# Kernel optimization log

Measured on AMD Instinct MI355X. Metric: run time of the kernel, lower is better.

Reference implementation:

```python
import math
import jax, jax.numpy as jnp
import numpy as np

D_MODEL = 1024
D_STATE = 16
D_CONV = 4
EXPAND = 2
D_INNER = EXPAND * D_MODEL
DT_RANK = max(1, math.ceil(D_MODEL / 16))
B_SZ, L_SEQ = 2, 2048


def setup_inputs() -> dict:
    key = jax.random.key(0)
    ks = jax.random.split(key, 8)
    s = 0.02
    x = jax.random.normal(ks[0], (B_SZ, L_SEQ, D_MODEL), dtype=jnp.float32)
    W_in = jax.random.normal(ks[1], (2 * D_INNER, D_MODEL), dtype=jnp.float32) * s
    conv_w = jax.random.normal(ks[2], (D_INNER, 1, D_CONV), dtype=jnp.float32) * s
    conv_b = jax.random.normal(ks[3], (D_INNER,), dtype=jnp.float32) * s
    W_xproj = jax.random.normal(ks[4], (DT_RANK + 2 * D_STATE, D_INNER), dtype=jnp.float32) * s
    W_dt = jax.random.normal(ks[5], (D_INNER, DT_RANK), dtype=jnp.float32) * s
    b_dt = jax.random.normal(ks[6], (D_INNER,), dtype=jnp.float32) * s
    A_log = jnp.broadcast_to(jnp.log(jnp.arange(1, D_STATE + 1, dtype=jnp.float32))[None, :], (D_INNER, D_STATE))
    D = jnp.ones((D_INNER,), dtype=jnp.float32)
    W_out = jax.random.normal(ks[7], (D_MODEL, D_INNER), dtype=jnp.float32) * s
    return {"x": x, "W_in": W_in, "conv_w": conv_w, "conv_b": conv_b,
            "W_xproj": W_xproj, "W_dt": W_dt, "b_dt": b_dt,
            "A_log": A_log, "D": D, "W_out": W_out}


def _silu(v):
    return v * jax.nn.sigmoid(v)


def _selective_scan(xc, dt, A, Bm, Cm):
    # xc, dt: (B, L, d_inner); A: (d_inner, N); Bm, Cm: (B, L, N)
    batch = xc.shape[0]
    h0 = jnp.zeros((batch, D_INNER, D_STATE), dtype=xc.dtype)

    def step(h, inp):
        x_t, dt_t, B_t, C_t = inp  # (B,d_inner), (B,d_inner), (B,N), (B,N)
        A_bar = jnp.exp(dt_t[:, :, None] * A[None])            # (B, d_inner, N)
        h = A_bar * h + (dt_t * x_t)[:, :, None] * B_t[:, None, :]
        y_t = jnp.einsum('bdn,bn->bd', h, C_t)
        return h, y_t

    xs = (jnp.swapaxes(xc, 0, 1), jnp.swapaxes(dt, 0, 1),
          jnp.swapaxes(Bm, 0, 1), jnp.swapaxes(Cm, 0, 1))
    _, ys = jax.lax.scan(step, h0, xs)  # ys: (L, B, d_inner)
    return jnp.swapaxes(ys, 0, 1)


def reference(x, W_in, conv_w, conv_b, W_xproj, W_dt, b_dt, A_log, D, W_out):
    # in_proj
    xz = jnp.einsum('bld,ed->ble', x, W_in)                    # (B, L, 2*d_inner)
    xc, z = jnp.split(xz, 2, axis=-1)
    # causal depthwise conv1d (torch pads d_conv-1 both sides then truncates to L)
    xc_ncl = jnp.swapaxes(xc, 1, 2)                            # (B, d_inner, L)
    xc_ncl = jax.lax.conv_general_dilated(
        xc_ncl, conv_w, window_strides=(1,), padding=[(D_CONV - 1, 0)],
        dimension_numbers=('NCH', 'OIH', 'NCH'), feature_group_count=D_INNER)
    xc_ncl = xc_ncl + conv_b[None, :, None]
    xc = _silu(jnp.swapaxes(xc_ncl, 1, 2))                     # (B, L, d_inner)
    # input-dependent dt, B, C
    xp = jnp.einsum('bld,ed->ble', xc, W_xproj)
    dt_lr = xp[:, :, :DT_RANK]
    Bm = xp[:, :, DT_RANK:DT_RANK + D_STATE]
    Cm = xp[:, :, DT_RANK + D_STATE:]
    dt = jax.nn.softplus(jnp.einsum('blr,dr->bld', dt_lr, W_dt) + b_dt)
    A = -jnp.exp(A_log)                                        # (d_inner, N)
    y = _selective_scan(xc, dt, A, Bm, Cm)
    y = y + xc * D[None, None, :]
    y = y * _silu(z)
    return jnp.einsum('bld,od->blo', y, W_out)
```

## Files before the change

kernel.cpp:

```cpp
#include <hip/hip_runtime.h>
#include <cstddef>
#include <cstdint>

#define DMODEL 1024
#define DI     2048
#define LSEQ   2048
#define NB     2
#define DSTATE 16
#define DTRANK 64
#define NXP    96
#define MROWS  (NB*LSEQ)
#define CHUNKS 32
#define LC     (LSEQ/CHUNKS)

typedef __attribute__((ext_vector_type(8))) short bf16x8;
typedef __attribute__((ext_vector_type(8))) unsigned short u16x8;
typedef __attribute__((ext_vector_type(4))) float f32x4;

__device__ __forceinline__ float silu_f(float v) {
  return v / (1.f + __expf(-v));
}
__device__ __forceinline__ float softplus_f(float v) {
  return (v > 20.f) ? v : log1pf(__expf(v));
}
__device__ __forceinline__ unsigned short f2bf(float f) {
  unsigned u = __float_as_uint(f);
  unsigned r = (u + 0x7FFFu + ((u >> 16) & 1u)) >> 16;
  return (unsigned short)r;
}
__device__ __forceinline__ float bf2f(unsigned short h) {
  return __uint_as_float(((unsigned)h) << 16);
}
__device__ __forceinline__ void gl2lds16(const void* g, void* l) {
  __builtin_amdgcn_global_load_lds(
      (const __attribute__((address_space(1))) void*)g,
      (__attribute__((address_space(3))) void*)l, 16, 0, 0);
}

__global__ __launch_bounds__(256)
void prep_kernel(const float* __restrict__ W_in, const float* __restrict__ W_dt,
                 const float* __restrict__ W_out, const float* __restrict__ x,
                 const float* __restrict__ W_xproj,
                 unsigned short* __restrict__ Whi, unsigned short* __restrict__ Wlo,
                 unsigned short* __restrict__ wdhi, unsigned short* __restrict__ wdlo,
                 unsigned short* __restrict__ Wohi, unsigned short* __restrict__ Wolo,
                 unsigned short* __restrict__ xhi, unsigned short* __restrict__ xlo,
                 unsigned short* __restrict__ wxhi, unsigned short* __restrict__ wxlo,
                 float* __restrict__ xp, float* __restrict__ out) {
  const int N_WIN  = 2*DI*DMODEL/4;
  const int N_WDT  = DI*DTRANK/4;
  const int N_WOUT = DMODEL*DI/4;
  const int N_X    = MROWS*DMODEL/4;
  const int N_WX   = 128*DI/4;
  const int N_XP   = MROWS*NXP/4;
  const int N_OUT  = MROWS*DMODEL/4;
  int i = blockIdx.x * 256 + threadIdx.x;
  const float* src = nullptr;
  unsigned short *hi = nullptr, *lo = nullptr;
  if (i < N_WIN)  { src = W_in;  hi = Whi;  lo = Wlo;  }
  else {
    i -= N_WIN;
    if (i < N_WDT)  { src = W_dt;  hi = wdhi; lo = wdlo; }
    else {
      i -= N_WDT;
      if (i < N_WOUT) { src = W_out; hi = Wohi; lo = Wolo; }
      else {
        i -= N_WOUT;
        if (i < N_X) { src = x; hi = xhi; lo = xlo; }
        else {
          i -= N_X;
          if (i < N_WX) {
            const int row = (i << 2) >> 11;
            float4 v = make_float4(0.f, 0.f, 0.f, 0.f);
            if (row < NXP) v = ((const float4*)W_xproj)[i];
            ushort4 h, l;
            h.x = f2bf(v.x); h.y = f2bf(v.y); h.z = f2bf(v.z); h.w = f2bf(v.w);
            l.x = f2bf(v.x - bf2f(h.x)); l.y = f2bf(v.y - bf2f(h.y));
            l.z = f2bf(v.z - bf2f(h.z)); l.w = f2bf(v.w - bf2f(h.w));
            ((ushort4*)wxhi)[i] = h; ((ushort4*)wxlo)[i] = l;
            return;
          }
          i -= N_WX;
          if (i < N_XP) { ((float4*)xp)[i] = make_float4(0.f,0.f,0.f,0.f); }
          else {
            i -= N_XP;
            if (i < N_OUT) ((float4*)out)[i] = make_float4(0.f,0.f,0.f,0.f);
          }
          return;
        }
      }
    }
  }
  float4 v = ((const float4*)src)[i];
  ushort4 h, l;
  h.x = f2bf(v.x); h.y = f2bf(v.y); h.z = f2bf(v.z); h.w = f2bf(v.w);
  l.x = f2bf(v.x - bf2f(h.x)); l.y = f2bf(v.y - bf2f(h.y));
  l.z = f2bf(v.z - bf2f(h.z)); l.w = f2bf(v.w - bf2f(h.w));
  ((ushort4*)hi)[i] = h; ((ushort4*)lo)[i] = l;
}

__global__ __launch_bounds__(256)
void dt_gemm_kernel(const float* __restrict__ xp_,
                    const unsigned short* __restrict__ wdhi,
                    const unsigned short* __restrict__ wdlo,
                    const float* __restrict__ bias,
                    float* __restrict__ dtb_) {
  const int tid  = threadIdx.x;
  const int lane = tid & 63;
  const int wv   = tid >> 6;
  const int wm   = wv >> 1, wn = wv & 1;
  const int quad = lane >> 4, lr = lane & 15;
  const int bm = blockIdx.y * 128, bn = blockIdx.x * 128;

  f32x4 acc[4][4];
  #pragma unroll
  for (int i = 0; i < 4; ++i)
    #pragma unroll
    for (int j = 0; j < 4; ++j)
      acc[i][j] = (f32x4){0.f, 0.f, 0.f, 0.f};

  #pragma unroll
  for (int kk = 0; kk < 2; ++kk) {
    const int k0 = kk * 32 + quad * 8;
    bf16x8 ah[4], al[4], bh[4], bl[4];
    #pragma unroll
    for (int i = 0; i < 4; ++i) {
      const int row = bm + wm * 64 + i * 16 + lr;
      const float* ap = xp_ + (size_t)row * NXP + k0;
      const float4 v0 = *(const float4*)ap;
      const float4 v1 = *(const float4*)(ap + 4);
      const float av[8] = {v0.x, v0.y, v0.z, v0.w, v1.x, v1.y, v1.z, v1.w};
      bf16x8 h, l;
      #pragma unroll
      for (int e = 0; e < 8; ++e) {
        const float v = av[e];
        const unsigned u = __float_as_uint(v);
        const float rem = v - __uint_as_float(u & 0xFFFF0000u);
        h[e] = (short)(u >> 16);
        l[e] = (short)(__float_as_uint(rem) >> 16);
      }
      ah[i] = h; al[i] = l;
    }
    #pragma unroll
    for (int j = 0; j < 4; ++j) {
      const int col = bn + wn * 64 + j * 16 + lr;
      bh[j] = *(const bf16x8*)(wdhi + (size_t)col * DTRANK + k0);
      bl[j] = *(const bf16x8*)(wdlo + (size_t)col * DTRANK + k0);
    }
    #pragma unroll
    for (int i = 0; i < 4; ++i)
      #pragma unroll
      for (int j = 0; j < 4; ++j) {
        acc[i][j] = __builtin_amdgcn_mfma_f32_16x16x32_bf16(ah[i], bh[j], acc[i][j], 0, 0, 0);
        acc[i][j] = __builtin_amdgcn_mfma_f32_16x16x32_bf16(ah[i], bl[j], acc[i][j], 0, 0, 0);
        acc[i][j] = __builtin_amdgcn_mfma_f32_16x16x32_bf16(al[i], bh[j], acc[i][j], 0, 0, 0);
      }
  }

  #pragma unroll
  for (int i = 0; i < 4; ++i) {
    const int gr = bm + wm * 64 + i * 16 + quad * 4;
    #pragma unroll
    for (int j = 0; j < 4; ++j) {
      const int gc = bn + wn * 64 + j * 16 + lr;
      float* cp = dtb_ + (size_t)gr * DI + gc;
      const float bv = bias[gc];
      #pragma unroll
      for (int r = 0; r < 4; ++r)
        cp[(size_t)r * DI] = softplus_f(acc[i][j][r] + bv);
    }
  }
}

template<bool ATOMIC, int ACT, bool APRE>
__device__ __forceinline__
void gemm_body(const float* __restrict__ A,
               const unsigned short* __restrict__ Ahi_g,
               const unsigned short* __restrict__ Alo_g,
               int lda,
               const unsigned short* __restrict__ Bhi, const unsigned short* __restrict__ Blo,
               const float* __restrict__ bias,
               float* __restrict__ C0, float* __restrict__ C1,
               int NC, int K, int klen) {
  __shared__ __align__(16) unsigned short Ah[2 * 128 * 32];
  __shared__ __align__(16) unsigned short Al[2 * 128 * 32];
  __shared__ __align__(16) unsigned short Bh[2 * 128 * 32];
  __shared__ __align__(16) unsigned short Bl[2 * 128 * 32];
  const int tid  = threadIdx.x;
  const int lane = tid & 63;
  const int wv   = tid >> 6;
  const int wm   = wv >> 1, wn = wv & 1;
  const int quad = lane >> 4, lr = lane & 15;
  const int bm = blockIdx.y * 128, bn = blockIdx.x * 128;
  const int kbeg = blockIdx.z * klen;

  int bOff[2], aOffp[2], ldsO[2];
  #pragma unroll
  for (int j = 0; j < 2; ++j) {
    const int s   = (wv * 2 + j) * 64 + lane;
    const int row = s >> 2;
    const int c   = (s & 3) ^ ((row >> 1) & 3);
    bOff[j]  = (bn + row) * K + c * 8;
    aOffp[j] = (bm + row) * lda + c * 8;
    ldsO[j]  = (wv * 2 + j) << 10;
  }
  const int ar = tid >> 1;
  const int ahalf = tid & 1;
  const int asw = (ar >> 1) & 3;
  const int aw0 = (ar * 4 + ((ahalf * 2)     ^ asw)) << 4;
  const int aw1 = (ar * 4 + ((ahalf * 2 + 1) ^ asw)) << 4;
  const float* aptr = (!APRE) ? (A + (size_t)(bm + ar) * lda + ahalf * 16) : nullptr;

  int aRd[4], bRd[4];
  #pragma unroll
  for (int i = 0; i < 4; ++i) {
    const int ra = wm * 64 + i * 16 + lr;
    aRd[i] = (ra * 4 + (quad ^ ((ra >> 1) & 3))) << 4;
    const int rb = wn * 64 + i * 16 + lr;
    bRd[i] = (rb * 4 + (quad ^ ((rb >> 1) & 3))) << 4;
  }

  f32x4 acc[4][4];
  #pragma unroll
  for (int i = 0; i < 4; ++i)
    #pragma unroll
    for (int j = 0; j < 4; ++j)
      acc[i][j] = (f32x4){0.f, 0.f, 0.f, 0.f};

  const int nt = klen / 32;
  float ac[16], an[16];

  if constexpr (APRE) {
    #pragma unroll
    for (int j = 0; j < 2; ++j) {
      gl2lds16(Bhi   + (size_t)bOff[j]  + kbeg, (char*)Bh + ldsO[j]);
      gl2lds16(Blo   + (size_t)bOff[j]  + kbeg, (char*)Bl + ldsO[j]);
      gl2lds16(Ahi_g + (size_t)aOffp[j] + kbeg, (char*)Ah + ldsO[j]);
      gl2lds16(Alo_g + (size_t)aOffp[j] + kbeg, (char*)Al + ldsO[j]);
    }
  } else {
    #pragma unroll
    for (int j = 0; j < 2; ++j) {
      gl2lds16(Bhi + (size_t)bOff[j] + kbeg, (char*)Bh + ldsO[j]);
      gl2lds16(Blo + (size_t)bOff[j] + kbeg, (char*)Bl + ldsO[j]);
    }
    #pragma unroll
    for (int q = 0; q < 4; ++q)
      *(float4*)&ac[q * 4] = *(const float4*)(aptr + kbeg + q * 4);
    u16x8 vh[2], vl[2];
    #pragma unroll
    for (int g = 0; g < 2; ++g)
      #pragma unroll
      for (int e = 0; e < 8; ++e) {
        const float v = ac[g * 8 + e];
        const unsigned u = __float_as_uint(v);
        const float rem = v - __uint_as_float(u & 0xFFFF0000u);
        vh[g][e] = (unsigned short)(u >> 16);
        vl[g][e] = (unsigned short)(__float_as_uint(rem) >> 16);
      }
    *(u16x8*)((char*)Ah + aw0) = vh[0];
    *(u16x8*)((char*)Ah + aw1) = vh[1];
    *(u16x8*)((char*)Al + aw0) = vl[0];
    *(u16x8*)((char*)Al + aw1) = vl[1];
    if (nt > 1) {
      #pragma unroll
      for (int q = 0; q < 4; ++q)
        *(float4*)&ac[q * 4] = *(const float4*)(aptr + kbeg + 32 + q * 4);
    }
  }
  asm volatile("s_waitcnt vmcnt(0)" ::: "memory");
  __syncthreads();

  int cur = 0;
  #pragma unroll 1
  for (int t = 0; t < nt; ++t) {
    const int km = kbeg + t * 32;
    if (t + 1 < nt) {
      const int nb = (cur ^ 1) * 8192;
      if constexpr (APRE) {
        #pragma unroll
        for (int j = 0; j < 2; ++j) {
          gl2lds16(Bhi   + (size_t)bOff[j]  + km + 32, (char*)Bh + nb + ldsO[j]);
          gl2lds16(Blo   + (size_t)bOff[j]  + km + 32, (char*)Bl + nb + ldsO[j]);
          gl2lds16(Ahi_g + (size_t)aOffp[j] + km + 32, (char*)Ah + nb + ldsO[j]);
          gl2lds16(Alo_g + (size_t)aOffp[j] + km + 32, (char*)Al + nb + ldsO[j]);
        }
      } else {
        #pragma unroll
        for (int j = 0; j < 2; ++j) {
          gl2lds16(Bhi + (size_t)bOff[j] + km + 32, (char*)Bh + nb + ldsO[j]);
          gl2lds16(Blo + (size_t)bOff[j] + km + 32, (char*)Bl + nb + ldsO[j]);
        }
        u16x8 vh[2], vl[2];
        #pragma unroll
        for (int g = 0; g < 2; ++g)
          #pragma unroll
          for (int e = 0; e < 8; ++e) {
            const float v = ac[g * 8 + e];
            const unsigned u = __float_as_uint(v);
            const float rem = v - __uint_as_float(u & 0xFFFF0000u);
            vh[g][e] = (unsigned short)(u >> 16);
            vl[g][e] = (unsigned short)(__float_as_uint(rem) >> 16);
          }
        *(u16x8*)((char*)Ah + nb + aw0) = vh[0];
        *(u16x8*)((char*)Ah + nb + aw1) = vh[1];
        *(u16x8*)((char*)Al + nb + aw0) = vl[0];
        *(u16x8*)((char*)Al + nb + aw1) = vl[1];
        if (t + 2 < nt) {
          #pragma unroll
          for (int q = 0; q < 4; ++q)
            *(float4*)&an[q * 4] = *(const float4*)(aptr + km + 64 + q * 4);
        }
      }
    }
    const int cb = cur * 8192;
    bf16x8 ah[4], al[4], bh[4], bl[4];
    #pragma unroll
    for (int i = 0; i < 4; ++i) {
      ah[i] = *(const bf16x8*)((const char*)Ah + cb + aRd[i]);
      al[i] = *(const bf16x8*)((const char*)Al + cb + aRd[i]);
      bh[i] = *(const bf16x8*)((const char*)Bh + cb + bRd[i]);
      bl[i] = *(const bf16x8*)((const char*)Bl + cb + bRd[i]);
    }
    #pragma unroll
    for (int i = 0; i < 4; ++i)
      #pragma unroll
      for (int j = 0; j < 4; ++j) {
        acc[i][j] = __builtin_amdgcn_mfma_f32_16x16x32_bf16(ah[i], bh[j], acc[i][j], 0, 0, 0);
        acc[i][j] = __builtin_amdgcn_mfma_f32_16x16x32_bf16(ah[i], bl[j], acc[i][j], 0, 0, 0);
        acc[i][j] = __builtin_amdgcn_mfma_f32_16x16x32_bf16(al[i], bh[j], acc[i][j], 0, 0, 0);
      }
    if (t + 1 < nt) {
      asm volatile("s_waitcnt vmcnt(0)" ::: "memory");
      __syncthreads();
      if constexpr (!APRE) {
        if (t + 2 < nt) {
          #pragma unroll
          for (int e = 0; e < 16; ++e) ac[e] = an[e];
        }
      }
      cur ^= 1;
    }
  }

  float* C = C0;
  int bnc = bn;
  if (bn >= NC) { C = C1; bnc = bn - NC; }

  #pragma unroll
  for (int i = 0; i < 4; ++i) {
    const int gr = bm + wm * 64 + i * 16 + quad * 4;
    #pragma unroll
    for (int j = 0; j < 4; ++j) {
      const int gc = bnc + wn * 64 + j * 16 + lr;
      float* cp = C + (size_t)gr * NC + gc;
      const float bv = (ACT == 1) ? bias[gc] : 0.f;
      #pragma unroll
      for (int r = 0; r < 4; ++r) {
        float v = acc[i][j][r];
        if (ACT == 1) v = softplus_f(v + bv);
        if (ATOMIC) atomicAdd(&cp[(size_t)r * NC], v);
        else        cp[(size_t)r * NC] = v;
      }
    }
  }
}

__global__ __launch_bounds__(256)
void gemm_in_bf16x3(const unsigned short* __restrict__ Ahi_g,
                    const unsigned short* __restrict__ Alo_g, int lda,
                    const unsigned short* __restrict__ Bhi,
                    const unsigned short* __restrict__ Blo,
                    float* __restrict__ C0, float* __restrict__ C1,
                    int NC, int K, int klen) {
  gemm_body<false, 0, true>(nullptr, Ahi_g, Alo_g, lda, Bhi, Blo, nullptr,
                            C0, C1, NC, K, klen);
}

__global__ __launch_bounds__(256)
void gemm_out_bf16x3(const float* __restrict__ A, int lda,
                     const unsigned short* __restrict__ Bhi,
                     const unsigned short* __restrict__ Blo,
                     float* __restrict__ C0,
                     int NC, int K, int klen) {
  gemm_body<true, 0, false>(A, nullptr, nullptr, lda, Bhi, Blo, nullptr,
                            C0, C0, NC, K, klen);
}

__global__ __launch_bounds__(256)
void xproj_gemm_bf16x3(const unsigned short* __restrict__ Ahi_g,
                       const unsigned short* __restrict__ Alo_g,
                       const unsigned short* __restrict__ Bhi,
                       const unsigned short* __restrict__ Blo,
                       float* __restrict__ C, int klen) {
  __shared__ __align__(16) unsigned short Ah[2 * 128 * 32];
  __shared__ __align__(16) unsigned short Al[2 * 128 * 32];
  __shared__ __align__(16) unsigned short Bh[2 * 128 * 32];
  __shared__ __align__(16) unsigned short Bl[2 * 128 * 32];
  const int tid  = threadIdx.x;
  const int lane = tid & 63;
  const int wv   = tid >> 6;
  const int wm   = wv >> 1, wn = wv & 1;
  const int quad = lane >> 4, lr = lane & 15;
  const int bm = blockIdx.y * 128;
  const int kbeg = blockIdx.z * klen;

  int bOff[2], aOff[2], ldsO[2];
  #pragma unroll
  for (int j = 0; j < 2; ++j) {
    const int s   = (wv * 2 + j) * 64 + lane;
    const int row = s >> 2;
    const int c   = (s & 3) ^ ((row >> 1) & 3);
    bOff[j] = row * DI + c * 8;
    aOff[j] = (bm + row) * DI + c * 8;
    ldsO[j] = (wv * 2 + j) << 10;
  }
  int aRd[4], bRd[4];
  #pragma unroll
  for (int i = 0; i < 4; ++i) {
    const int ra = wm * 64 + i * 16 + lr;
    aRd[i] = (ra * 4 + (quad ^ ((ra >> 1) & 3))) << 4;
    const int rb = wn * 64 + i * 16 + lr;
    bRd[i] = (rb * 4 + (quad ^ ((rb >> 1) & 3))) << 4;
  }

  f32x4 acc[4][4];
  #pragma unroll
  for (int i = 0; i < 4; ++i)
    #pragma unroll
    for (int j = 0; j < 4; ++j)
      acc[i][j] = (f32x4){0.f, 0.f, 0.f, 0.f};

  const int nt = klen / 32;
  #pragma unroll
  for (int j = 0; j < 2; ++j) {
    gl2lds16(Ahi_g + (size_t)aOff[j] + kbeg, (char*)Ah + ldsO[j]);
    gl2lds16(Alo_g + (size_t)aOff[j] + kbeg, (char*)Al + ldsO[j]);
    gl2lds16(Bhi   + (size_t)bOff[j] + kbeg, (char*)Bh + ldsO[j]);
    gl2lds16(Blo   + (size_t)bOff[j] + kbeg, (char*)Bl + ldsO[j]);
  }
  asm volatile("s_waitcnt vmcnt(0)" ::: "memory");
  __syncthreads();

  int cur = 0;
  #pragma unroll 1
  for (int t = 0; t < nt; ++t) {
    const int km = kbeg + t * 32;
    if (t + 1 < nt) {
      const int nb = (cur ^ 1) * 8192;
      #pragma unroll
      for (int j = 0; j < 2; ++j) {
        gl2lds16(Ahi_g + (size_t)aOff[j] + km + 32, (char*)Ah + nb + ldsO[j]);
        gl2lds16(Alo_g + (size_t)aOff[j] + km + 32, (char*)Al + nb + ldsO[j]);
        gl2lds16(Bhi   + (size_t)bOff[j] + km + 32, (char*)Bh + nb + ldsO[j]);
        gl2lds16(Blo   + (size_t)bOff[j] + km + 32, (char*)Bl + nb + ldsO[j]);
      }
    }
    const int cb = cur * 8192;
    bf16x8 ah[4], al[4], bh[4], bl[4];
    #pragma unroll
    for (int i = 0; i < 4; ++i) {
      ah[i] = *(const bf16x8*)((const char*)Ah + cb + aRd[i]);
      al[i] = *(const bf16x8*)((const char*)Al + cb + aRd[i]);
      bh[i] = *(const bf16x8*)((const char*)Bh + cb + bRd[i]);
      bl[i] = *(const bf16x8*)((const char*)Bl + cb + bRd[i]);
    }
    #pragma unroll
    for (int i = 0; i < 4; ++i)
      #pragma unroll
      for (int j = 0; j < 4; ++j) {
        acc[i][j] = __builtin_amdgcn_mfma_f32_16x16x32_bf16(ah[i], bh[j], acc[i][j], 0, 0, 0);
        acc[i][j] = __builtin_amdgcn_mfma_f32_16x16x32_bf16(ah[i], bl[j], acc[i][j], 0, 0, 0);
        acc[i][j] = __builtin_amdgcn_mfma_f32_16x16x32_bf16(al[i], bh[j], acc[i][j], 0, 0, 0);
      }
    if (t + 1 < nt) {
      asm volatile("s_waitcnt vmcnt(0)" ::: "memory");
      __syncthreads();
      cur ^= 1;
    }
  }

  #pragma unroll
  for (int i = 0; i < 4; ++i) {
    const int gr = bm + wm * 64 + i * 16 + quad * 4;
    #pragma unroll
    for (int j = 0; j < 4; ++j) {
      const int gc = wn * 64 + j * 16 + lr;
      if (gc < NXP) {
        float* cp = C + (size_t)gr * NXP + gc;
        #pragma unroll
        for (int r = 0; r < 4; ++r)
          atomicAdd(&cp[(size_t)r * NXP], acc[i][j][r]);
      }
    }
  }
}

__global__ __launch_bounds__(256)
void conv_silu_kernel(const float* __restrict__ xc_raw, const float* __restrict__ cw,
                      const float* __restrict__ cb, float* __restrict__ xc2,
                      unsigned short* __restrict__ xc2hi,
                      unsigned short* __restrict__ xc2lo) {
  const int tid = blockIdx.x * 256 + threadIdx.x;
  const int d4 = tid & (DI / 4 - 1);
  const int l  = (tid >> 9) & (LSEQ - 1);
  const int b  = tid >> 20;
  const size_t rowb = ((size_t)b * LSEQ + l) * DI + d4 * 4;
  float4 xj[4];
  #pragma unroll
  for (int j = 0; j < 4; ++j) {
    const int ls = l - 3 + j;
    xj[j] = (ls >= 0) ? *(const float4*)(xc_raw + rowb + ((long long)j - 3) * DI)
                      : make_float4(0.f, 0.f, 0.f, 0.f);
  }
  const float4 bias = *(const float4*)(cb + d4 * 4);
  float o[4];
  #pragma unroll
  for (int k = 0; k < 4; ++k) {
    const float4 w = *(const float4*)(cw + (d4 * 4 + k) * 4);
    const float xv[4] = { ((const float*)&xj[0])[k], ((const float*)&xj[1])[k],
                          ((const float*)&xj[2])[k], ((const float*)&xj[3])[k] };
    float acc = fmaf(w.x, xv[0], ((const float*)&bias)[k]);
    acc = fmaf(w.y, xv[1], acc);
    acc = fmaf(w.z, xv[2], acc);
    acc = fmaf(w.w, xv[3], acc);
    o[k] = silu_f(acc);
  }
  *(float4*)(xc2 + rowb) = make_float4(o[0], o[1], o[2], o[3]);
  ushort4 h, lo4;
  h.x = f2bf(o[0]); h.y = f2bf(o[1]); h.z = f2bf(o[2]); h.w = f2bf(o[3]);
  lo4.x = f2bf(o[0] - bf2f(h.x)); lo4.y = f2bf(o[1] - bf2f(h.y));
  lo4.z = f2bf(o[2] - bf2f(h.z)); lo4.w = f2bf(o[3] - bf2f(h.w));
  *(ushort4*)(xc2hi + rowb) = h;
  *(ushort4*)(xc2lo + rowb) = lo4;
}

__global__ __launch_bounds__(256)
void scan_chunk_kernel(const float* __restrict__ xc2, float* __restrict__ dtb,
                       const float* __restrict__ xp, const float* __restrict__ A_log,
                       float* __restrict__ y_local, float* __restrict__ hloc,
                       float* __restrict__ totdt) {
  __shared__ float sbc[LC][32];
  const int d = blockIdx.x * 256 + threadIdx.x;
  const int b = blockIdx.y;
  const int c = blockIdx.z;

  float A[DSTATE], h[DSTATE];
  #pragma unroll
  for (int n = 0; n < DSTATE; ++n) {
    A[n] = -__expf(A_log[(size_t)d * DSTATE + n]);
    h[n] = 0.f;
  }

  const float* xpb = xp + ((size_t)b * LSEQ + (size_t)c * LC) * NXP + DTRANK;
  #pragma unroll
  for (int kk = 0; kk < 2; ++kk) {
    const int slot = threadIdx.x + kk * 256;
    const int row = slot >> 3, c4 = (slot & 7) << 2;
    *(float4*)&sbc[row][c4] = *(const float4*)&xpb[(size_t)row * NXP + c4];
  }
  __syncthreads();

  const size_t cbase = ((size_t)b * LSEQ + (size_t)c * LC) * DI + d;
  float cum = 0.f;
  constexpr int U = 4;
  float cdt[U], cx[U];
  #pragma unroll
  for (int u = 0; u < U; ++u) {
    cdt[u] = dtb[cbase + (size_t)u * DI];
    cx[u]  = xc2[cbase + (size_t)u * DI];
  }

  #pragma unroll 1
  for (int g = 0; g < LC; g += U) {
    float ndt[U], nx[U];
    if (g + U < LC) {
      #pragma unroll
      for (int u = 0; u < U; ++u) {
        ndt[u] = dtb[cbase + (size_t)(g + U + u) * DI];
        nx[u]  = xc2[cbase + (size_t)(g + U + u) * DI];
      }
    }
    #pragma unroll
    for (int u = 0; u < U; ++u) {
      const int t = g + u;
      const float dt = cdt[u];
      const float dx = dt * cx[u];
      cum += dt;
      #pragma unroll
      for (int n = 0; n < DSTATE; ++n) {
        const float ab = __expf(dt * A[n]);
        h[n] = fmaf(ab, h[n], dx * sbc[t][n]);
      }
      float p[DSTATE];
      #pragma unroll
      for (int n = 0; n < DSTATE; ++n) p[n] = h[n] * sbc[t][DSTATE + n];
      #pragma unroll
      for (int s = 1; s < DSTATE; s <<= 1)
        #pragma unroll
        for (int n = 0; n < DSTATE; n += 2 * s) p[n] += p[n + s];
      const size_t base = cbase + (size_t)t * DI;
      y_local[base] = p[0];
      dtb[base] = cum;
    }
    if (g + U < LC) {
      #pragma unroll
      for (int u = 0; u < U; ++u) { cdt[u] = ndt[u]; cx[u] = nx[u]; }
    }
  }

  const size_t hbase = ((size_t)(b * CHUNKS + c)) * DSTATE * DI + d;
  #pragma unroll
  for (int n = 0; n < DSTATE; ++n) hloc[hbase + (size_t)n * DI] = h[n];
  totdt[((size_t)(b * CHUNKS + c)) * DI + d] = cum;
}

__global__ __launch_bounds__(256)
void scan_carry_kernel(float* __restrict__ hloc, const float* __restrict__ totdt,
                       const float* __restrict__ A_log) {
  const int tid = blockIdx.x * 256 + threadIdx.x;
  const int d = tid & (DI - 1);
  const int n = (tid >> 11) & 15;
  const int b = tid >> 15;
  const float An = -__expf(A_log[(size_t)d * DSTATE + n]);
  float h = 0.f;
  float le = hloc[((size_t)(b * CHUNKS) * DSTATE + n) * DI + d];
  float td = totdt[(size_t)(b * CHUNKS) * DI + d];
  for (int c = 0; c < CHUNKS; ++c) {
    const size_t ix = ((size_t)(b * CHUNKS + c) * DSTATE + n) * DI + d;
    float nle = 0.f, ntd = 0.f;
    if (c + 1 < CHUNKS) {
      nle = hloc[ix + (size_t)DSTATE * DI];
      ntd = totdt[(size_t)(b * CHUNKS + c + 1) * DI + d];
    }
    hloc[ix] = h;
    h = fmaf(__expf(An * td), h, le);
    le = nle; td = ntd;
  }
}

__global__ __launch_bounds__(256)
void scan_fix_kernel(const float* __restrict__ xc2, const float* __restrict__ dtb,
                     const float* __restrict__ xp, const float* __restrict__ zbuf,
                     const float* __restrict__ A_log, const float* __restrict__ Dp,
                     const float* __restrict__ hloc, float* __restrict__ y) {
  __shared__ float sC[LC][DSTATE];
  const int tid = threadIdx.x;
  const int d = blockIdx.x * 256 + tid;
  const int b = blockIdx.y;
  const int c = blockIdx.z;

  {
    const float* xpc = xp + ((size_t)b * LSEQ + (size_t)c * LC) * NXP + DTRANK + DSTATE;
    const int row = tid >> 2, q = tid & 3;
    *(float4*)&sC[row][q * 4] = *(const float4*)&xpc[(size_t)row * NXP + q * 4];
  }

  float Ar[DSTATE], hr[DSTATE];
  {
    const float* hp = hloc + ((size_t)(b * CHUNKS + c)) * DSTATE * DI + d;
    const float* ap = A_log + (size_t)d * DSTATE;
    #pragma unroll
    for (int n = 0; n < DSTATE; ++n) {
      Ar[n] = -__expf(ap[n]);
      hr[n] = hp[(size_t)n * DI];
    }
  }
  __syncthreads();

  const float Dd = Dp[d];
  const size_t base = ((size_t)b * LSEQ + (size_t)c * LC) * DI + d;

  float cum = dtb[base], xv = xc2[base], zv = zbuf[base], yv = y[base];
  #pragma unroll 1
  for (int lt = 0; lt < LC; ++lt) {
    const size_t idx = base + (size_t)lt * DI;
    float cumN = 0.f, xvN = 0.f, zvN = 0.f, yvN = 0.f;
    if (lt + 1 < LC) {
      const size_t ix1 = idx + DI;
      cumN = dtb[ix1]; xvN = xc2[ix1]; zvN = zbuf[ix1]; yvN = y[ix1];
    }
    float corr = 0.f;
    #pragma unroll
    for (int n = 0; n < DSTATE; ++n)
      corr = fmaf(__expf(Ar[n] * cum) * hr[n], sC[lt][n], corr);
    y[idx] = (yv + corr + xv * Dd) * silu_f(zv);
    cum = cumN; xv = xvN; zv = zvN; yv = yvN;
  }
}

extern "C" void kernel_launch(void* const* d_in, const int* in_sizes, int n_in,
                              void* d_out, int out_size, void* d_ws, size_t ws_size,
                              hipStream_t stream) {
  const float* x      = (const float*)d_in[0];
  const float* W_in   = (const float*)d_in[1];
  const float* conv_w = (const float*)d_in[2];
  const float* conv_b = (const float*)d_in[3];
  const float* W_xproj= (const float*)d_in[4];
  const float* W_dt   = (const float*)d_in[5];
  const float* b_dt   = (const float*)d_in[6];
  const float* A_log  = (const float*)d_in[7];
  const float* Dp     = (const float*)d_in[8];
  const float* W_out  = (const float*)d_in[9];
  float* out = (float*)d_out;
  float* ws  = (float*)d_ws;

  const size_t SEG = (size_t)NB * LSEQ * DI;
  float* xc_raw = ws;
  float* zbuf   = ws + SEG;
  float* xc2    = ws + 2 * SEG;
  float* dtb    = ws + 3 * SEG;
  float* xp     = ws + 4 * SEG;
  float* hloc   = xp + (size_t)MROWS * NXP;
  float* totdt  = hloc + (size_t)NB * CHUNKS * DSTATE * DI;
  float* wpool  = totdt + (size_t)NB * CHUNKS * DI;

  unsigned short* Whi = (unsigned short*)dtb;
  unsigned short* Wlo = Whi + (size_t)2 * DI * DMODEL;

  unsigned short* xc2hi = (unsigned short*)dtb;
  unsigned short* xc2lo = xc2hi + (size_t)MROWS * DI;

  unsigned short* xhi = (unsigned short*)xc2;
  unsigned short* xlo = xhi + (size_t)MROWS * DMODEL;

  unsigned short* Wohi = (unsigned short*)wpool;
  unsigned short* Wolo = Wohi + (size_t)DMODEL * DI;
  unsigned short* wdhi = Wolo + (size_t)DMODEL * DI;
  unsigned short* wdlo = wdhi + (size_t)DI * DTRANK;
  unsigned short* wxhi = wdlo + (size_t)DI * DTRANK;
  unsigned short* wxlo = wxhi + (size_t)128 * DI;

  float* yb = xc_raw;
  dim3 blk(256);

  const int prep_blocks = (2*DI*DMODEL/4 + DI*DTRANK/4 + DMODEL*DI/4
                           + MROWS*DMODEL/4 + 128*DI/4
                           + MROWS*NXP/4 + MROWS*DMODEL/4) / 256;
  prep_kernel<<<prep_blocks, blk, 0, stream>>>(
      W_in, W_dt, W_out, x, W_xproj, Whi, Wlo, wdhi, wdlo, Wohi, Wolo,
      xhi, xlo, wxhi, wxlo, xp, out);

  gemm_in_bf16x3<<<dim3(2*DI/128, MROWS/128, 1), blk, 0, stream>>>(
      xhi, xlo, DMODEL, Whi, Wlo, xc_raw, zbuf, DI, DMODEL, DMODEL);

  conv_silu_kernel<<<(NB*LSEQ*(DI/4))/256, blk, 0, stream>>>(
      xc_raw, conv_w, conv_b, xc2, xc2hi, xc2lo);

  xproj_gemm_bf16x3<<<dim3(1, MROWS/128, 8), blk, 0, stream>>>(
      xc2hi, xc2lo, wxhi, wxlo, xp, DI/8);

  dt_gemm_kernel<<<dim3(DI/128, MROWS/128, 1), blk, 0, stream>>>(
      xp, wdhi, wdlo, b_dt, dtb);

  scan_chunk_kernel<<<dim3(DI/256, NB, CHUNKS), blk, 0, stream>>>(
      xc2, dtb, xp, A_log, yb, hloc, totdt);
  scan_carry_kernel<<<(NB*DI*DSTATE)/256, blk, 0, stream>>>(hloc, totdt, A_log);
  scan_fix_kernel<<<dim3(DI/256, NB, CHUNKS), blk, 0, stream>>>(
      xc2, dtb, xp, zbuf, A_log, Dp, hloc, yb);

  gemm_out_bf16x3<<<dim3(DMODEL/128, MROWS/128, 2), blk, 0, stream>>>(
      yb, DI, Wohi, Wolo, out, DMODEL, DI, DI/2);
}
```

Before: 452.2 us.

## Rescan chunks from carried state and emit bf16 hi/lo y for out-proj

The first scan pass now only computes the chunk-final local states and total dt, with no per-step y or cumulative-dt writes. A new final pass reruns the recurrence from the true carried-in state. Within that pass it computes y with the D skip and SiLU(z) gate and writes it directly as bf16 hi/lo pairs, so the output GEMM reads pre-split operands instead of converting fp32 on the fly. This removes the exp-based correction term and several global reads and writes, but it recomputes the recurrence a second time.

```diff
diff --git a/kernel.cpp b/kernel.cpp
--- a/kernel.cpp
+++ b/kernel.cpp
@@ -378,13 +378,14 @@
 }
 
 __global__ __launch_bounds__(256)
-void gemm_out_bf16x3(const float* __restrict__ A, int lda,
+void gemm_out_bf16x3(const unsigned short* __restrict__ Ahi_g,
+                     const unsigned short* __restrict__ Alo_g, int lda,
                      const unsigned short* __restrict__ Bhi,
                      const unsigned short* __restrict__ Blo,
                      float* __restrict__ C0,
                      int NC, int K, int klen) {
-  gemm_body<true, 0, false>(A, nullptr, nullptr, lda, Bhi, Blo, nullptr,
-                            C0, C0, NC, K, klen);
+  gemm_body<true, 0, true>(nullptr, Ahi_g, Alo_g, lda, Bhi, Blo, nullptr,
+                           C0, C0, NC, K, klen);
 }
 
 __global__ __launch_bounds__(256)
@@ -536,11 +537,10 @@
 }
 
 __global__ __launch_bounds__(256)
-void scan_chunk_kernel(const float* __restrict__ xc2, float* __restrict__ dtb,
+void scan_chunk_kernel(const float* __restrict__ xc2, const float* __restrict__ dtb,
                        const float* __restrict__ xp, const float* __restrict__ A_log,
-                       float* __restrict__ y_local, float* __restrict__ hloc,
-                       float* __restrict__ totdt) {
-  __shared__ float sbc[LC][32];
+                       float* __restrict__ hloc, float* __restrict__ totdt) {
+  __shared__ float sB[LC][DSTATE];
   const int d = blockIdx.x * 256 + threadIdx.x;
   const int b = blockIdx.y;
   const int c = blockIdx.z;
@@ -552,12 +552,10 @@
     h[n] = 0.f;
   }
 
-  const float* xpb = xp + ((size_t)b * LSEQ + (size_t)c * LC) * NXP + DTRANK;
-  #pragma unroll
-  for (int kk = 0; kk < 2; ++kk) {
-    const int slot = threadIdx.x + kk * 256;
-    const int row = slot >> 3, c4 = (slot & 7) << 2;
-    *(float4*)&sbc[row][c4] = *(const float4*)&xpb[(size_t)row * NXP + c4];
+  {
+    const float* xpb = xp + ((size_t)b * LSEQ + (size_t)c * LC) * NXP + DTRANK;
+    const int row = threadIdx.x >> 2, q = threadIdx.x & 3;
+    *(float4*)&sB[row][q * 4] = *(const float4*)&xpb[(size_t)row * NXP + q * 4];
   }
   __syncthreads();
 
@@ -590,18 +588,8 @@
       #pragma unroll
       for (int n = 0; n < DSTATE; ++n) {
         const float ab = __expf(dt * A[n]);
-        h[n] = fmaf(ab, h[n], dx * sbc[t][n]);
-      }
-      float p[DSTATE];
-      #pragma unroll
-      for (int n = 0; n < DSTATE; ++n) p[n] = h[n] * sbc[t][DSTATE + n];
-      #pragma unroll
-      for (int s = 1; s < DSTATE; s <<= 1)
-        #pragma unroll
-        for (int n = 0; n < DSTATE; n += 2 * s) p[n] += p[n + s];
-      const size_t base = cbase + (size_t)t * DI;
-      y_local[base] = p[0];
-      dtb[base] = cum;
+        h[n] = fmaf(ab, h[n], dx * sB[t][n]);
+      }
     }
     if (g + U < LC) {
       #pragma unroll
@@ -640,52 +628,88 @@
 }
 
 __global__ __launch_bounds__(256)
-void scan_fix_kernel(const float* __restrict__ xc2, const float* __restrict__ dtb,
-                     const float* __restrict__ xp, const float* __restrict__ zbuf,
-                     const float* __restrict__ A_log, const float* __restrict__ Dp,
-                     const float* __restrict__ hloc, float* __restrict__ y) {
-  __shared__ float sC[LC][DSTATE];
+void scan_final_kernel(const float* __restrict__ xc2, const float* __restrict__ dtb,
+                       const float* __restrict__ xp, const float* __restrict__ zbuf,
+                       const float* __restrict__ A_log, const float* __restrict__ Dp,
+                       const float* __restrict__ hloc,
+                       unsigned short* __restrict__ yhi,
+                       unsigned short* __restrict__ ylo) {
+  __shared__ float sbc[LC][32];
   const int tid = threadIdx.x;
   const int d = blockIdx.x * 256 + tid;
   const int b = blockIdx.y;
   const int c = blockIdx.z;
 
-  {
-    const float* xpc = xp + ((size_t)b * LSEQ + (size_t)c * LC) * NXP + DTRANK + DSTATE;
-    const int row = tid >> 2, q = tid & 3;
-    *(float4*)&sC[row][q * 4] = *(const float4*)&xpc[(size_t)row * NXP + q * 4];
-  }
-
-  float Ar[DSTATE], hr[DSTATE];
+  float A[DSTATE], h[DSTATE];
   {
     const float* hp = hloc + ((size_t)(b * CHUNKS + c)) * DSTATE * DI + d;
     const float* ap = A_log + (size_t)d * DSTATE;
     #pragma unroll
     for (int n = 0; n < DSTATE; ++n) {
-      Ar[n] = -__expf(ap[n]);
-      hr[n] = hp[(size_t)n * DI];
+      A[n] = -__expf(ap[n]);
+      h[n] = hp[(size_t)n * DI];
+    }
+  }
+  {
+    const float* xpb = xp + ((size_t)b * LSEQ + (size_t)c * LC) * NXP + DTRANK;
+    #pragma unroll
+    for (int kk = 0; kk < 2; ++kk) {
+      const int slot = tid + kk * 256;
+      const int row = slot >> 3, q4 = (slot & 7) << 2;
+      *(float4*)&sbc[row][q4] = *(const float4*)&xpb[(size_t)row * NXP + q4];
     }
   }
   __syncthreads();
 
   const float Dd = Dp[d];
-  const size_t base = ((size_t)b * LSEQ + (size_t)c * LC) * DI + d;
-
-  float cum = dtb[base], xv = xc2[base], zv = zbuf[base], yv = y[base];
+  const size_t cbase = ((size_t)b * LSEQ + (size_t)c * LC) * DI + d;
+  constexpr int U = 4;
+  float cdt[U], cx[U], cz[U];
+  #pragma unroll
+  for (int u = 0; u < U; ++u) {
+    cdt[u] = dtb[cbase + (size_t)u * DI];
+    cx[u]  = xc2[cbase + (size_t)u * DI];
+    cz[u]  = zbuf[cbase + (size_t)u * DI];
+  }
+
   #pragma unroll 1
-  for (int lt = 0; lt < LC; ++lt) {
-    const size_t idx = base + (size_t)lt * DI;
-    float cumN = 0.f, xvN = 0.f, zvN = 0.f, yvN = 0.f;
-    if (lt + 1 < LC) {
-      const size_t ix1 = idx + DI;
-      cumN = dtb[ix1]; xvN = xc2[ix1]; zvN = zbuf[ix1]; yvN = y[ix1];
-    }
-    float corr = 0.f;
-    #pragma unroll
-    for (int n = 0; n < DSTATE; ++n)
-      corr = fmaf(__expf(Ar[n] * cum) * hr[n], sC[lt][n], corr);
-    y[idx] = (yv + corr + xv * Dd) * silu_f(zv);
-    cum = cumN; xv = xvN; zv = zvN; yv = yvN;
+  for (int g = 0; g < LC; g += U) {
+    float ndt[U], nx[U], nz[U];
+    if (g + U < LC) {
+      #pragma unroll
+      for (int u = 0; u < U; ++u) {
+        ndt[u] = dtb[cbase + (size_t)(g + U + u) * DI];
+        nx[u]  = xc2[cbase + (size_t)(g + U + u) * DI];
+        nz[u]  = zbuf[cbase + (size_t)(g + U + u) * DI];
+      }
+    }
+    #pragma unroll
+    for (int u = 0; u < U; ++u) {
+      const int t = g + u;
+      const float dt = cdt[u];
+      const float dx = dt * cx[u];
+      #pragma unroll
+      for (int n = 0; n < DSTATE; ++n) {
+        const float ab = __expf(dt * A[n]);
+        h[n] = fmaf(ab, h[n], dx * sbc[t][n]);
+      }
+      float p[DSTATE];
+      #pragma unroll
+      for (int n = 0; n < DSTATE; ++n) p[n] = h[n] * sbc[t][DSTATE + n];
+      #pragma unroll
+      for (int s = 1; s < DSTATE; s <<= 1)
+        #pragma unroll
+        for (int n = 0; n < DSTATE; n += 2 * s) p[n] += p[n + s];
+      const float yv = (p[0] + cx[u] * Dd) * silu_f(cz[u]);
+      const size_t base = cbase + (size_t)t * DI;
+      const unsigned short hh = f2bf(yv);
+      yhi[base] = hh;
+      ylo[base] = f2bf(yv - bf2f(hh));
+    }
+    if (g + U < LC) {
+      #pragma unroll
+      for (int u = 0; u < U; ++u) { cdt[u] = ndt[u]; cx[u] = nx[u]; cz[u] = nz[u]; }
+    }
   }
 }
 
@@ -724,6 +748,9 @@
   unsigned short* xhi = (unsigned short*)xc2;
   unsigned short* xlo = xhi + (size_t)MROWS * DMODEL;
 
+  unsigned short* yhi = (unsigned short*)xc_raw;
+  unsigned short* ylo = yhi + (size_t)MROWS * DI;
+
   unsigned short* Wohi = (unsigned short*)wpool;
   unsigned short* Wolo = Wohi + (size_t)DMODEL * DI;
   unsigned short* wdhi = Wolo + (size_t)DMODEL * DI;
@@ -731,7 +758,6 @@
   unsigned short* wxhi = wdlo + (size_t)DI * DTRANK;
   unsigned short* wxlo = wxhi + (size_t)128 * DI;
 
-  float* yb = xc_raw;
   dim3 blk(256);
 
   const int prep_blocks = (2*DI*DMODEL/4 + DI*DTRANK/4 + DMODEL*DI/4
@@ -754,11 +780,11 @@
       xp, wdhi, wdlo, b_dt, dtb);
 
   scan_chunk_kernel<<<dim3(DI/256, NB, CHUNKS), blk, 0, stream>>>(
-      xc2, dtb, xp, A_log, yb, hloc, totdt);
+      xc2, dtb, xp, A_log, hloc, totdt);
   scan_carry_kernel<<<(NB*DI*DSTATE)/256, blk, 0, stream>>>(hloc, totdt, A_log);
-  scan_fix_kernel<<<dim3(DI/256, NB, CHUNKS), blk, 0, stream>>>(
-      xc2, dtb, xp, zbuf, A_log, Dp, hloc, yb);
+  scan_final_kernel<<<dim3(DI/256, NB, CHUNKS), blk, 0, stream>>>(
+      xc2, dtb, xp, zbuf, A_log, Dp, hloc, yhi, ylo);
 
   gemm_out_bf16x3<<<dim3(DMODEL/128, MROWS/128, 2), blk, 0, stream>>>(
-      yb, DI, Wohi, Wolo, out, DMODEL, DI, DI/2);
-}
+      yhi, ylo, DI, Wohi, Wolo, out, DMODEL, DI, DI/2);
+}
```

Measured after the change: 430.4 us. 4.8% less time.
